# Performance work log

Measured on AMD Instinct MI355X. Metric: run time of the kernel, lower is better.

## Reference

```python
import jax, jax.numpy as jnp
import numpy as np

H, K, D = 4096, 16, 256  # hidden_dim, num_slots, slot_dim
BOT = 512                # decoder bottleneck
N_ITER = 3
EPS = 1e-5


def _ln(x, g, b):
    mu = jnp.mean(x, axis=-1, keepdims=True)
    var = jnp.var(x, axis=-1, keepdims=True)
    return (x - mu) * jax.lax.rsqrt(var + EPS) * g + b


def setup_inputs() -> dict:
    key = jax.random.key(0)
    ks = jax.random.split(key, 24)
    r = lambda i, shape, s=0.02: jax.random.normal(ks[i], shape, jnp.float32) * s
    inp = {
        "hidden_states": jax.random.normal(ks[0], (8, 4096, H), jnp.float32),
        "old_slots": jax.random.normal(ks[1], (8, K, D), jnp.float32) * 0.02,
        # SlotAttention params
        "in_w": r(2, (H, D)), "in_b": jnp.zeros((D,), jnp.float32),
        "ln_in_g": jnp.ones((D,), jnp.float32), "ln_in_b": jnp.zeros((D,), jnp.float32),
        "ln_s_g": jnp.ones((D,), jnp.float32), "ln_s_b": jnp.zeros((D,), jnp.float32),
        "ln_m_g": jnp.ones((D,), jnp.float32), "ln_m_b": jnp.zeros((D,), jnp.float32),
        "q_w": r(3, (D, D)), "k_w": r(4, (D, D)), "v_w": r(5, (D, D)),
        "mlp_w1": r(6, (D, 2 * D)), "mlp_b1": jnp.zeros((2 * D,), jnp.float32),
        "mlp_w2": r(7, (2 * D, D)), "mlp_b2": jnp.zeros((D,), jnp.float32),
        # ReconstructionDecoder params
        "dec_w1": r(8, (D, BOT)), "dec_b1": jnp.zeros((BOT,), jnp.float32),
        "dec_w2": r(9, (BOT, BOT)), "dec_b2": jnp.zeros((BOT,), jnp.float32),
        "dec_w3": r(10, (BOT, H)), "dec_b3": jnp.zeros((H,), jnp.float32),
    }
    return inp


def _forward(hidden_states, old_slots, in_w, in_b, ln_in_g, ln_in_b, ln_s_g, ln_s_b,
             ln_m_g, ln_m_b, q_w, k_w, v_w, mlp_w1, mlp_b1, mlp_w2, mlp_b2,
             dec_w1, dec_b1, dec_w2, dec_b2, dec_w3, dec_b3):
    B, T, _ = hidden_states.shape
    # subsample: 256 linspace over front + last 256 tokens (T > 512 branch)
    idx_front = jnp.linspace(0.0, T - 256, 256).astype(jnp.int32)  # torch long cast truncates; values are exact floor here
    idx_back = jnp.arange(T - 256, T, dtype=jnp.int32)
    idx = jnp.concatenate([idx_front, idx_back])
    sampled = hidden_states[:, idx, :]                 # [B, 512, H]

    x = _ln(sampled @ in_w + in_b, ln_in_g, ln_in_b)   # [B, 512, D]
    k = x @ k_w                                        # [B, 512, D]
    v = x @ v_w
    scale = D ** (-0.5)

    slots = old_slots                                  # [B, K, D]
    for _ in range(N_ITER):
        s = _ln(slots, ln_s_g, ln_s_b)
        q = s @ q_w
        logits = jnp.einsum('bkd,bnd->bkn', q, k) * scale
        attn = jax.nn.softmax(logits, axis=1)          # softmax over SLOT axis
        upd = jnp.einsum('bkn,bnd->bkd', attn, v)
        h = _ln(upd, ln_m_g, ln_m_b)
        slots = s + jax.nn.gelu(h @ mlp_w1 + mlp_b1, approximate=False) @ mlp_w2 + mlp_b2

    # reconstruction loss
    target = jax.lax.stop_gradient(jnp.mean(hidden_states, axis=1))     # [B, H]
    r = jax.nn.gelu(slots @ dec_w1 + dec_b1, approximate=False)
    r = jax.nn.gelu(r @ dec_w2 + dec_b2, approximate=False)
    r = r @ dec_w3 + dec_b3                                             # [B, K, H]
    recon = jnp.mean(r, axis=1)                                         # [B, H]
    recon_loss = jnp.mean((recon - target) ** 2)
    return slots, recon_loss


def reference(hidden_states, old_slots, in_w, in_b, ln_in_g, ln_in_b, ln_s_g, ln_s_b,
              ln_m_g, ln_m_b, q_w, k_w, v_w, mlp_w1, mlp_b1, mlp_w2, mlp_b2,
              dec_w1, dec_b1, dec_w2, dec_b2, dec_w3, dec_b3):
    return _forward(hidden_states, old_slots, in_w, in_b, ln_in_g, ln_in_b, ln_s_g,
                    ln_s_b, ln_m_g, ln_m_b, q_w, k_w, v_w, mlp_w1, mlp_b1, mlp_w2,
                    mlp_b2, dec_w1, dec_b1, dec_w2, dec_b2, dec_w3, dec_b3)
```

## Files before the change

kernel.cpp:

```cpp
#include <hip/hip_runtime.h>

typedef unsigned short u16;
typedef float f32x4 __attribute__((ext_vector_type(4)));
typedef __bf16 bf16x8 __attribute__((ext_vector_type(8)));
typedef u16 u16x4 __attribute__((ext_vector_type(4)));

__device__ __forceinline__ u16 f2bf(float f){
  union { float f; unsigned u; } x; x.f = f;
  return (u16)((x.u + 0x7FFFu + ((x.u >> 16) & 1u)) >> 16);
}
__device__ __forceinline__ float bf2f(u16 s){
  union { unsigned u; float f; } x; x.u = ((unsigned)s) << 16;
  return x.f;
}
__device__ __forceinline__ f32x4 mfma16(bf16x8 a, bf16x8 b, f32x4 c){
  return __builtin_amdgcn_mfma_f32_16x16x32_bf16(a, b, c, 0, 0, 0);
}
__device__ __forceinline__ float wred_sum(float x){
  #pragma unroll
  for (int m = 1; m < 64; m <<= 1) x += __shfl_xor(x, m);
  return x;
}
__device__ __forceinline__ float gelu_f(float v){
  return 0.5f * v * (1.0f + erff(v * 0.70710678118654752440f));
}
__device__ __forceinline__ int sample_idx(int r){
  return (r < 256) ? (3840 * r) / 255 : (3584 + r);
}

__global__ __launch_bounds__(256) void k_prep(
    const float* __restrict__ in_w, const float* __restrict__ q_w,
    const float* __restrict__ k_w, const float* __restrict__ v_w,
    const float* __restrict__ w1, const float* __restrict__ w2,
    u16* __restrict__ in_wT, u16* __restrict__ q_wT, u16* __restrict__ k_wT,
    u16* __restrict__ v_wT, u16* __restrict__ w1T, u16* __restrict__ w2T,
    float* __restrict__ loss_slot)
{
  __shared__ float tile[64][65];
  int id = blockIdx.x;
  const float* src; u16* dst; int R, C, t;
  if (id < 256)      { src=in_w; dst=in_wT; R=4096; C=256; t=id; }
  else if (id < 272) { src=q_w;  dst=q_wT;  R=256;  C=256; t=id-256; }
  else if (id < 288) { src=k_w;  dst=k_wT;  R=256;  C=256; t=id-272; }
  else if (id < 304) { src=v_w;  dst=v_wT;  R=256;  C=256; t=id-288; }
  else if (id < 336) { src=w1;   dst=w1T;   R=256;  C=512; t=id-304; }
  else               { src=w2;   dst=w2T;   R=512;  C=256; t=id-336; }
  int tC = C >> 6;
  int r0 = (t / tC) * 64, c0 = (t % tC) * 64;
  int tr = threadIdx.x >> 6, tc = threadIdx.x & 63;
  #pragma unroll
  for (int rr = tr; rr < 64; rr += 4)
    tile[rr][tc] = src[(size_t)(r0+rr)*C + c0 + tc];
  __syncthreads();
  #pragma unroll
  for (int cc = tr; cc < 64; cc += 4)
    dst[(size_t)(c0+cc)*R + r0 + tc] = f2bf(tile[tc][cc]);
  if (id == 0 && threadIdx.x == 0) *loss_slot = 0.f;
}

__global__ __launch_bounds__(256) void k_colsum(const float* __restrict__ hs,
                                                float* __restrict__ parts)
{
  int tc = blockIdx.x;
  int hb = blockIdx.y;
  int b  = blockIdx.z;
  int h0 = hb*1024 + threadIdx.x*4;
  const float* p = hs + ((size_t)b*4096 + (size_t)tc*64)*4096 + h0;
  f32x4 s = {0.f,0.f,0.f,0.f};
  for (int t = 0; t < 64; ++t)
    s += *reinterpret_cast<const f32x4*>(p + (size_t)t*4096);
  *reinterpret_cast<f32x4*>(parts + ((size_t)(b*64+tc) << 12) + h0) = s;
}

__global__ __launch_bounds__(256) void k_colsum2(const float* __restrict__ parts,
                                                 float* __restrict__ tgt)
{
  int i = blockIdx.x*256 + threadIdx.x;
  int b = i >> 12, h = i & 4095;
  float s = 0.f;
  for (int c = 0; c < 64; ++c) s += parts[((size_t)(b*64+c) << 12) + h];
  tgt[i] = s * (1.0f/4096.0f);
}

__global__ __launch_bounds__(256) void k_in_gemm_ln(
    const float* __restrict__ hs, const u16* __restrict__ in_wT,
    const float* __restrict__ in_b,
    const float* __restrict__ ln_g, const float* __restrict__ ln_b,
    u16* __restrict__ x_b)
{
  __shared__ float xt[16][260];
  const int lane = threadIdx.x & 63;
  const int w = threadIdx.x >> 6;
  const int c16 = lane & 15, g4 = lane >> 4;
  const int m0 = blockIdx.x * 16;
  const int row = m0 + c16;
  const int b = row >> 9;
  const int tok = row & 511;
  const int src = sample_idx(tok);
  const float* arow = hs + ((size_t)b*4096 + src)*4096 + g4*8;

  f32x4 acc[4];
  #pragma unroll
  for (int ct=0; ct<4; ++ct) acc[ct] = (f32x4){0.f,0.f,0.f,0.f};

  for (int k0 = 0; k0 < 4096; k0 += 32) {
    f32x4 a0 = *reinterpret_cast<const f32x4*>(arow + k0);
    f32x4 a1 = *reinterpret_cast<const f32x4*>(arow + k0 + 4);
    union { u16 u[8]; bf16x8 v; } af;
    #pragma unroll
    for (int i=0;i<4;++i){ af.u[i] = f2bf(a0[i]); af.u[4+i] = f2bf(a1[i]); }
    #pragma unroll
    for (int ct=0; ct<4; ++ct){
      int col = w*64 + ct*16 + c16;
      bf16x8 bf = *reinterpret_cast<const bf16x8*>(in_wT + (size_t)col*4096 + k0 + g4*8);
      acc[ct] = mfma16(af.v, bf, acc[ct]);
    }
  }
  #pragma unroll
  for (int ct=0; ct<4; ++ct){
    int col = w*64 + ct*16 + c16;
    float bias = in_b[col];
    #pragma unroll
    for (int i=0;i<4;++i) xt[g4*4+i][col] = acc[ct][i] + bias;
  }
  __syncthreads();
  #pragma unroll
  for (int rr=0; rr<4; ++rr){
    int r = 4*w + rr;
    f32x4 v = *reinterpret_cast<const f32x4*>(&xt[r][4*lane]);
    float s = v[0]+v[1]+v[2]+v[3];
    float q = v[0]*v[0]+v[1]*v[1]+v[2]*v[2]+v[3]*v[3];
    s = wred_sum(s); q = wred_sum(q);
    float mu = s*(1.0f/256.0f);
    float var = q*(1.0f/256.0f) - mu*mu;
    float rs = rsqrtf(var + 1e-5f);
    u16x4 pk;
    #pragma unroll
    for (int i=0;i<4;++i) pk[i] = f2bf((v[i]-mu)*rs*ln_g[4*lane+i] + ln_b[4*lane+i]);
    *reinterpret_cast<u16x4*>(x_b + (size_t)(m0 + r)*256 + 4*lane) = pk;
  }
}

__global__ __launch_bounds__(256) void k_kv(
    const u16* __restrict__ x_b, const u16* __restrict__ k_wT, const u16* __restrict__ v_wT,
    u16* __restrict__ k_out, u16* __restrict__ vT_out)
{
  const int lane = threadIdx.x & 63;
  const int w = threadIdx.x >> 6;
  const int c16 = lane & 15, g4 = lane >> 4;
  const int m0 = blockIdx.x * 16;
  const u16* aptr = x_b + (size_t)(m0 + c16)*256 + g4*8;
  f32x4 ak[4], av[4];
  #pragma unroll
  for (int ct=0; ct<4; ++ct){ ak[ct]=(f32x4){0.f,0.f,0.f,0.f}; av[ct]=(f32x4){0.f,0.f,0.f,0.f}; }
  #pragma unroll
  for (int kk=0; kk<8; ++kk){
    bf16x8 af = *reinterpret_cast<const bf16x8*>(aptr + kk*32);
    #pragma unroll
    for (int ct=0; ct<4; ++ct){
      int col = w*64 + ct*16 + c16;
      bf16x8 bk = *reinterpret_cast<const bf16x8*>(k_wT + (size_t)col*256 + kk*32 + g4*8);
      bf16x8 bv = *reinterpret_cast<const bf16x8*>(v_wT + (size_t)col*256 + kk*32 + g4*8);
      ak[ct] = mfma16(af, bk, ak[ct]);
      av[ct] = mfma16(af, bv, av[ct]);
    }
  }
  const int b = m0 >> 9;
  const int tok0 = (m0 & 511) + g4*4;
  #pragma unroll
  for (int ct=0; ct<4; ++ct){
    int col = w*64 + ct*16 + c16;
    #pragma unroll
    for (int i=0;i<4;++i)
      k_out[(size_t)(m0 + g4*4 + i)*256 + col] = f2bf(ak[ct][i]);
    u16x4 pk;
    #pragma unroll
    for (int i=0;i<4;++i) pk[i] = f2bf(av[ct][i]);
    *reinterpret_cast<u16x4*>(vT_out + ((size_t)(b*256 + col))*512 + tok0) = pk;
  }
}

__global__ __launch_bounds__(1024) void k_slots(
    const float* __restrict__ old_slots,
    const u16* __restrict__ k_b, const u16* __restrict__ vT_b,
    const u16* __restrict__ q_wT, const u16* __restrict__ w1T, const u16* __restrict__ w2T,
    const float* __restrict__ ln_s_g, const float* __restrict__ ln_s_b,
    const float* __restrict__ ln_m_g, const float* __restrict__ ln_m_b,
    const float* __restrict__ mlp_b1, const float* __restrict__ mlp_b2,
    float* __restrict__ out_slots)
{
  __shared__ u16 bufA[16*264];
  __shared__ u16 qS[16*264];
  __shared__ u16 wideS[16*520];
  __shared__ u16 updS[16*264];

  const int lane = threadIdx.x & 63;
  const int w    = threadIdx.x >> 6;
  const int c16  = lane & 15;
  const int g4   = lane >> 4;
  const int b    = blockIdx.x;

  const u16* kb = k_b  + (size_t)b * 512 * 256;
  const u16* vb = vT_b + (size_t)b * 256 * 512;

  float sl[4];
  {
    const float* p = old_slots + ((size_t)b*16 + w)*256 + 4*lane;
    #pragma unroll
    for (int i=0;i<4;++i) sl[i] = p[i];
  }
  float lsg[4], lsbv[4], lmg[4], lmb[4];
  #pragma unroll
  for (int i=0;i<4;++i){
    lsg[i]  = ln_s_g[4*lane+i];
    lsbv[i] = ln_s_b[4*lane+i];
    lmg[i]  = ln_m_g[4*lane+i];
    lmb[i]  = ln_m_b[4*lane+i];
  }
  const float b1a = mlp_b1[32*w + c16];
  const float b1b = mlp_b1[32*w + 16 + c16];
  const float b2c = mlp_b2[16*w + c16];
  float sv[4];

  for (int it = 0; it < 3; ++it) {
    {
      float s = sl[0]+sl[1]+sl[2]+sl[3];
      float q = sl[0]*sl[0]+sl[1]*sl[1]+sl[2]*sl[2]+sl[3]*sl[3];
      s = wred_sum(s); q = wred_sum(q);
      float mu = s * (1.0f/256.0f);
      float var = q * (1.0f/256.0f) - mu*mu;
      float rs = rsqrtf(var + 1e-5f);
      u16x4 pk;
      #pragma unroll
      for (int i=0;i<4;++i){ sv[i] = (sl[i]-mu)*rs*lsg[i] + lsbv[i]; pk[i] = f2bf(sv[i]); }
      *reinterpret_cast<u16x4*>(bufA + w*264 + 4*lane) = pk;
    }
    __syncthreads();

    {
      f32x4 acc = {0.f,0.f,0.f,0.f};
      #pragma unroll
      for (int kk = 0; kk < 8; ++kk) {
        bf16x8 af = *reinterpret_cast<const bf16x8*>(bufA + c16*264 + kk*32 + g4*8);
        bf16x8 bf = *reinterpret_cast<const bf16x8*>(q_wT + (size_t)(16*w + c16)*256 + kk*32 + g4*8);
        acc = mfma16(af, bf, acc);
      }
      #pragma unroll
      for (int i=0;i<4;++i) qS[(g4*4+i)*264 + 16*w + c16] = f2bf(acc[i]);
    }
    __syncthreads();

    {
      bf16x8 qf[8];
      #pragma unroll
      for (int kk=0;kk<8;++kk)
        qf[kk] = *reinterpret_cast<const bf16x8*>(qS + c16*264 + kk*32 + g4*8);
      #pragma unroll
      for (int ct=0; ct<2; ++ct) {
        int n0 = 32*w + 16*ct;
        f32x4 acc = {0.f,0.f,0.f,0.f};
        #pragma unroll
        for (int kk=0;kk<8;++kk){
          bf16x8 bf = *reinterpret_cast<const bf16x8*>(kb + (size_t)(n0 + c16)*256 + kk*32 + g4*8);
          acc = mfma16(qf[kk], bf, acc);
        }
        float t0 = acc[0]*0.0625f, t1 = acc[1]*0.0625f, t2 = acc[2]*0.0625f, t3 = acc[3]*0.0625f;
        float mx = fmaxf(fmaxf(t0,t1), fmaxf(t2,t3));
        mx = fmaxf(mx, __shfl_xor(mx,16));
        mx = fmaxf(mx, __shfl_xor(mx,32));
        float e0 = expf(t0-mx), e1 = expf(t1-mx), e2 = expf(t2-mx), e3 = expf(t3-mx);
        float ss = e0+e1+e2+e3;
        ss += __shfl_xor(ss,16);
        ss += __shfl_xor(ss,32);
        float inv = 1.0f/ss;
        wideS[(g4*4+0)*520 + n0 + c16] = f2bf(e0*inv);
        wideS[(g4*4+1)*520 + n0 + c16] = f2bf(e1*inv);
        wideS[(g4*4+2)*520 + n0 + c16] = f2bf(e2*inv);
        wideS[(g4*4+3)*520 + n0 + c16] = f2bf(e3*inv);
      }
    }
    __syncthreads();

    {
      f32x4 acc = {0.f,0.f,0.f,0.f};
      #pragma unroll
      for (int kk=0; kk<16; ++kk){
        bf16x8 af = *reinterpret_cast<const bf16x8*>(wideS + c16*520 + kk*32 + g4*8);
        bf16x8 bf = *reinterpret_cast<const bf16x8*>(vb + (size_t)(16*w + c16)*512 + kk*32 + g4*8);
        acc = mfma16(af, bf, acc);
      }
      #pragma unroll
      for (int i=0;i<4;++i) updS[(g4*4+i)*264 + 16*w + c16] = f2bf(acc[i]);
    }
    __syncthreads();

    {
      u16x4 up = *reinterpret_cast<const u16x4*>(updS + w*264 + 4*lane);
      float uv[4];
      #pragma unroll
      for (int i=0;i<4;++i) uv[i] = bf2f(up[i]);
      float s = uv[0]+uv[1]+uv[2]+uv[3];
      float q = uv[0]*uv[0]+uv[1]*uv[1]+uv[2]*uv[2]+uv[3]*uv[3];
      s = wred_sum(s); q = wred_sum(q);
      float mu = s*(1.0f/256.0f);
      float var = q*(1.0f/256.0f) - mu*mu;
      float rs = rsqrtf(var + 1e-5f);
      u16x4 pk;
      #pragma unroll
      for (int i=0;i<4;++i) pk[i] = f2bf((uv[i]-mu)*rs*lmg[i] + lmb[i]);
      *reinterpret_cast<u16x4*>(bufA + w*264 + 4*lane) = pk;
    }
    __syncthreads();

    {
      bf16x8 hf[8];
      #pragma unroll
      for (int kk=0;kk<8;++kk)
        hf[kk] = *reinterpret_cast<const bf16x8*>(bufA + c16*264 + kk*32 + g4*8);
      #pragma unroll
      for (int ct=0; ct<2; ++ct){
        int n0 = 32*w + 16*ct;
        float bb = ct ? b1b : b1a;
        f32x4 acc = {0.f,0.f,0.f,0.f};
        #pragma unroll
        for (int kk=0;kk<8;++kk){
          bf16x8 bf = *reinterpret_cast<const bf16x8*>(w1T + (size_t)(n0 + c16)*256 + kk*32 + g4*8);
          acc = mfma16(hf[kk], bf, acc);
        }
        #pragma unroll
        for (int i=0;i<4;++i)
          wideS[(g4*4+i)*520 + n0 + c16] = f2bf(gelu_f(acc[i] + bb));
      }
    }
    __syncthreads();

    {
      f32x4 acc = {0.f,0.f,0.f,0.f};
      #pragma unroll
      for (int kk=0; kk<16; ++kk){
        bf16x8 af = *reinterpret_cast<const bf16x8*>(wideS + c16*520 + kk*32 + g4*8);
        bf16x8 bf = *reinterpret_cast<const bf16x8*>(w2T + (size_t)(16*w + c16)*512 + kk*32 + g4*8);
        acc = mfma16(af, bf, acc);
      }
      #pragma unroll
      for (int i=0;i<4;++i) bufA[(g4*4+i)*264 + 16*w + c16] = f2bf(acc[i] + b2c);
    }
    __syncthreads();
    {
      u16x4 ns = *reinterpret_cast<const u16x4*>(bufA + w*264 + 4*lane);
      #pragma unroll
      for (int i=0;i<4;++i) sl[i] = sv[i] + bf2f(ns[i]);
    }
    __syncthreads();
  }

  {
    float* p = out_slots + ((size_t)b*16 + w)*256 + 4*lane;
    #pragma unroll
    for (int i=0;i<4;++i) p[i] = sl[i];
  }
}

__global__ __launch_bounds__(256) void k_dec(
    const float* __restrict__ slots, const float* __restrict__ w1, const float* __restrict__ b1,
    const float* __restrict__ w2, const float* __restrict__ b2, float* __restrict__ r2g)
{
  __shared__ float sr[256];
  __shared__ float r1[512];
  const int row = blockIdx.x;
  const int t = threadIdx.x;
  sr[t] = slots[(size_t)row*256 + t];
  __syncthreads();
  float a0 = b1[t], a1 = b1[t+256];
  for (int i=0;i<256;++i){
    float s = sr[i];
    a0 = fmaf(s, w1[(size_t)i*512 + t], a0);
    a1 = fmaf(s, w1[(size_t)i*512 + t + 256], a1);
  }
  r1[t] = gelu_f(a0); r1[t+256] = gelu_f(a1);
  __syncthreads();
  float c0 = b2[t], c1 = b2[t+256];
  for (int i=0;i<512;++i){
    float s = r1[i];
    c0 = fmaf(s, w2[(size_t)i*512 + t], c0);
    c1 = fmaf(s, w2[(size_t)i*512 + t + 256], c1);
  }
  r2g[(size_t)row*512 + t]       = gelu_f(c0);
  r2g[(size_t)row*512 + t + 256] = gelu_f(c1);
}

__global__ __launch_bounds__(256) void k_loss(
    const float* __restrict__ r2g, const float* __restrict__ w3, const float* __restrict__ b3,
    const float* __restrict__ tgt, float* __restrict__ loss)
{
  __shared__ float rb[512];
  __shared__ float red[4];
  const int hb = blockIdx.x;
  const int b  = blockIdx.y;
  const int t  = threadIdx.x;
  for (int j = t; j < 512; j += 256){
    float s = 0.f;
    #pragma unroll
    for (int k2=0;k2<16;++k2) s += r2g[(size_t)(b*16 + k2)*512 + j];
    rb[j] = s * (1.0f/16.0f);
  }
  __syncthreads();
  const int h = hb*1024 + t*4;
  f32x4 acc = *reinterpret_cast<const f32x4*>(b3 + h);
  for (int j=0;j<512;++j){
    f32x4 wv = *reinterpret_cast<const f32x4*>(w3 + (size_t)j*4096 + h);
    float rj = rb[j];
    acc[0] = fmaf(rj, wv[0], acc[0]);
    acc[1] = fmaf(rj, wv[1], acc[1]);
    acc[2] = fmaf(rj, wv[2], acc[2]);
    acc[3] = fmaf(rj, wv[3], acc[3]);
  }
  f32x4 tg = *reinterpret_cast<const f32x4*>(tgt + (size_t)b*4096 + h);
  float d0 = acc[0]-tg[0], d1 = acc[1]-tg[1], d2 = acc[2]-tg[2], d3 = acc[3]-tg[3];
  float loc = d0*d0 + d1*d1 + d2*d2 + d3*d3;
  loc = wred_sum(loc);
  const int lane = t & 63, wv_ = t >> 6;
  if (lane == 0) red[wv_] = loc;
  __syncthreads();
  if (t == 0){
    float s = (red[0]+red[1]+red[2]+red[3]) * (1.0f/32768.0f);
    atomicAdd(loss, s);
  }
}

extern "C" void kernel_launch(void* const* d_in, const int* in_sizes, int n_in,
                              void* d_out, int out_size, void* d_ws, size_t ws_size,
                              hipStream_t stream)
{
  const float* hs      = (const float*)d_in[0];
  const float* oslots  = (const float*)d_in[1];
  const float* in_w    = (const float*)d_in[2];
  const float* in_b    = (const float*)d_in[3];
  const float* ln_in_g = (const float*)d_in[4];
  const float* ln_in_b = (const float*)d_in[5];
  const float* ln_s_g  = (const float*)d_in[6];
  const float* ln_s_b  = (const float*)d_in[7];
  const float* ln_m_g  = (const float*)d_in[8];
  const float* ln_m_b  = (const float*)d_in[9];
  const float* q_w     = (const float*)d_in[10];
  const float* k_w     = (const float*)d_in[11];
  const float* v_w     = (const float*)d_in[12];
  const float* mlp_w1  = (const float*)d_in[13];
  const float* mlp_b1  = (const float*)d_in[14];
  const float* mlp_w2  = (const float*)d_in[15];
  const float* mlp_b2  = (const float*)d_in[16];
  const float* dec_w1  = (const float*)d_in[17];
  const float* dec_b1  = (const float*)d_in[18];
  const float* dec_w2  = (const float*)d_in[19];
  const float* dec_b2  = (const float*)d_in[20];
  const float* dec_w3  = (const float*)d_in[21];
  const float* dec_b3  = (const float*)d_in[22];

  char* ws = (char*)d_ws;
  size_t off = 0;
  auto alloc = [&](size_t bytes)->char*{
    char* p = ws + off; off = (off + bytes + 255) & ~(size_t)255; return p;
  };
  float* tgt   = (float*)alloc((size_t)32768*4);
  float* parts = (float*)alloc((size_t)8*64*4096*4);
  u16* in_wT = (u16*)alloc((size_t)256*4096*2);
  u16* q_wT  = (u16*)alloc((size_t)65536*2);
  u16* k_wT  = (u16*)alloc((size_t)65536*2);
  u16* v_wT  = (u16*)alloc((size_t)65536*2);
  u16* w1T   = (u16*)alloc((size_t)131072*2);
  u16* w2T   = (u16*)alloc((size_t)131072*2);
  u16* x_b   = (u16*)alloc((size_t)4096*256*2);
  u16* kk_b  = (u16*)alloc((size_t)4096*256*2);
  u16* vT_b  = (u16*)alloc((size_t)8*256*512*2);
  float* r2g = (float*)alloc((size_t)128*512*4);

  float* out_slots = (float*)d_out;
  float* out_loss  = out_slots + 32768;

  hipLaunchKernelGGL(k_prep, dim3(368), dim3(256), 0, stream,
      in_w, q_w, k_w, v_w, mlp_w1, mlp_w2, in_wT, q_wT, k_wT, v_wT, w1T, w2T, out_loss);
  hipLaunchKernelGGL(k_colsum, dim3(64,4,8), dim3(256), 0, stream, hs, parts);
  hipLaunchKernelGGL(k_colsum2, dim3(128), dim3(256), 0, stream, parts, tgt);
  hipLaunchKernelGGL(k_in_gemm_ln, dim3(256), dim3(256), 0, stream,
      hs, in_wT, in_b, ln_in_g, ln_in_b, x_b);
  hipLaunchKernelGGL(k_kv, dim3(256), dim3(256), 0, stream, x_b, k_wT, v_wT, kk_b, vT_b);
  hipLaunchKernelGGL(k_slots, dim3(8), dim3(1024), 0, stream,
      oslots, kk_b, vT_b, q_wT, w1T, w2T,
      ln_s_g, ln_s_b, ln_m_g, ln_m_b, mlp_b1, mlp_b2, out_slots);
  hipLaunchKernelGGL(k_dec, dim3(128), dim3(256), 0, stream,
      out_slots, dec_w1, dec_b1, dec_w2, dec_b2, r2g);
  hipLaunchKernelGGL(k_loss, dim3(4,8), dim3(256), 0, stream,
      r2g, dec_w3, dec_b3, tgt, out_loss);
}
```

Measured before the change: 1.079 ms.

## Widen input GEMM blocks, split loss GEMV over j, use native bf16 convert

The input projection kernel now runs 8 waves per block, each owning 32 output columns instead of 64, so more waves share the same A-row loads and latency is better hidden. The decoder-loss GEMV is split along the bottleneck dimension into 4 partial kernels (128 blocks instead of 32), followed by a separate reduction kernel that adds the partials and computes the squared error. f2bf now uses the compiler's native bf16 conversion instead of manual rounding. The cost is an extra launch and a partial buffer, and the rounding behaviour for NaN may differ slightly.

```diff
diff --git a/kernel.cpp b/kernel.cpp
--- a/kernel.cpp
+++ b/kernel.cpp
@@ -6,8 +6,9 @@
 typedef u16 u16x4 __attribute__((ext_vector_type(4)));
 
 __device__ __forceinline__ u16 f2bf(float f){
-  union { float f; unsigned u; } x; x.f = f;
-  return (u16)((x.u + 0x7FFFu + ((x.u >> 16) & 1u)) >> 16);
+  __bf16 h = (__bf16)f;
+  union { __bf16 h; u16 u; } x; x.h = h;
+  return x.u;
 }
 __device__ __forceinline__ float bf2f(u16 s){
   union { unsigned u; float f; } x; x.u = ((unsigned)s) << 16;
@@ -82,7 +83,7 @@
   tgt[i] = s * (1.0f/4096.0f);
 }
 
-__global__ __launch_bounds__(256) void k_in_gemm_ln(
+__global__ __launch_bounds__(512) void k_in_gemm_ln(
     const float* __restrict__ hs, const u16* __restrict__ in_wT,
     const float* __restrict__ in_b,
     const float* __restrict__ ln_g, const float* __restrict__ ln_b,
@@ -99,9 +100,9 @@
   const int src = sample_idx(tok);
   const float* arow = hs + ((size_t)b*4096 + src)*4096 + g4*8;
 
-  f32x4 acc[4];
-  #pragma unroll
-  for (int ct=0; ct<4; ++ct) acc[ct] = (f32x4){0.f,0.f,0.f,0.f};
+  f32x4 acc[2];
+  acc[0] = (f32x4){0.f,0.f,0.f,0.f};
+  acc[1] = (f32x4){0.f,0.f,0.f,0.f};
 
   for (int k0 = 0; k0 < 4096; k0 += 32) {
     f32x4 a0 = *reinterpret_cast<const f32x4*>(arow + k0);
@@ -110,23 +111,23 @@
     #pragma unroll
     for (int i=0;i<4;++i){ af.u[i] = f2bf(a0[i]); af.u[4+i] = f2bf(a1[i]); }
     #pragma unroll
-    for (int ct=0; ct<4; ++ct){
-      int col = w*64 + ct*16 + c16;
+    for (int ct=0; ct<2; ++ct){
+      int col = w*32 + ct*16 + c16;
       bf16x8 bf = *reinterpret_cast<const bf16x8*>(in_wT + (size_t)col*4096 + k0 + g4*8);
       acc[ct] = mfma16(af.v, bf, acc[ct]);
     }
   }
   #pragma unroll
-  for (int ct=0; ct<4; ++ct){
-    int col = w*64 + ct*16 + c16;
+  for (int ct=0; ct<2; ++ct){
+    int col = w*32 + ct*16 + c16;
     float bias = in_b[col];
     #pragma unroll
     for (int i=0;i<4;++i) xt[g4*4+i][col] = acc[ct][i] + bias;
   }
   __syncthreads();
   #pragma unroll
-  for (int rr=0; rr<4; ++rr){
-    int r = 4*w + rr;
+  for (int rr=0; rr<2; ++rr){
+    int r = 2*w + rr;
     f32x4 v = *reinterpret_cast<const f32x4*>(&xt[r][4*lane]);
     float s = v[0]+v[1]+v[2]+v[3];
     float q = v[0]*v[0]+v[1]*v[1]+v[2]*v[2]+v[3]*v[3];
@@ -389,40 +390,54 @@
   r2g[(size_t)row*512 + t + 256] = gelu_f(c1);
 }
 
-__global__ __launch_bounds__(256) void k_loss(
+__global__ __launch_bounds__(256) void k_loss_part(
     const float* __restrict__ r2g, const float* __restrict__ w3, const float* __restrict__ b3,
-    const float* __restrict__ tgt, float* __restrict__ loss)
-{
-  __shared__ float rb[512];
-  __shared__ float red[4];
+    float* __restrict__ rpart)
+{
+  __shared__ float rb[128];
   const int hb = blockIdx.x;
   const int b  = blockIdx.y;
+  const int jc = blockIdx.z;
   const int t  = threadIdx.x;
-  for (int j = t; j < 512; j += 256){
+  const int j0 = jc*128;
+  if (t < 128){
     float s = 0.f;
     #pragma unroll
-    for (int k2=0;k2<16;++k2) s += r2g[(size_t)(b*16 + k2)*512 + j];
-    rb[j] = s * (1.0f/16.0f);
+    for (int k2=0;k2<16;++k2) s += r2g[(size_t)(b*16 + k2)*512 + j0 + t];
+    rb[t] = s * (1.0f/16.0f);
   }
   __syncthreads();
   const int h = hb*1024 + t*4;
-  f32x4 acc = *reinterpret_cast<const f32x4*>(b3 + h);
-  for (int j=0;j<512;++j){
-    f32x4 wv = *reinterpret_cast<const f32x4*>(w3 + (size_t)j*4096 + h);
+  f32x4 acc;
+  if (jc == 0) acc = *reinterpret_cast<const f32x4*>(b3 + h);
+  else         acc = (f32x4){0.f,0.f,0.f,0.f};
+  for (int j=0;j<128;++j){
+    f32x4 wv = *reinterpret_cast<const f32x4*>(w3 + (size_t)(j0+j)*4096 + h);
     float rj = rb[j];
     acc[0] = fmaf(rj, wv[0], acc[0]);
     acc[1] = fmaf(rj, wv[1], acc[1]);
     acc[2] = fmaf(rj, wv[2], acc[2]);
     acc[3] = fmaf(rj, wv[3], acc[3]);
   }
-  f32x4 tg = *reinterpret_cast<const f32x4*>(tgt + (size_t)b*4096 + h);
-  float d0 = acc[0]-tg[0], d1 = acc[1]-tg[1], d2 = acc[2]-tg[2], d3 = acc[3]-tg[3];
-  float loc = d0*d0 + d1*d1 + d2*d2 + d3*d3;
-  loc = wred_sum(loc);
-  const int lane = t & 63, wv_ = t >> 6;
+  *reinterpret_cast<f32x4*>(rpart + (((size_t)jc*8 + b) << 12) + h) = acc;
+}
+
+__global__ __launch_bounds__(256) void k_loss_final(
+    const float* __restrict__ rpart, const float* __restrict__ tgt,
+    float* __restrict__ loss)
+{
+  __shared__ float red[4];
+  int i = blockIdx.x*256 + threadIdx.x;
+  int b = i >> 12, h = i & 4095;
+  float r = 0.f;
+  #pragma unroll
+  for (int jc=0; jc<4; ++jc) r += rpart[(((size_t)jc*8 + b) << 12) + h];
+  float d = r - tgt[i];
+  float loc = wred_sum(d*d);
+  const int lane = threadIdx.x & 63, wv_ = threadIdx.x >> 6;
   if (lane == 0) red[wv_] = loc;
   __syncthreads();
-  if (t == 0){
+  if (threadIdx.x == 0){
     float s = (red[0]+red[1]+red[2]+red[3]) * (1.0f/32768.0f);
     atomicAdd(loss, s);
   }
@@ -473,6 +488,7 @@
   u16* kk_b  = (u16*)alloc((size_t)4096*256*2);
   u16* vT_b  = (u16*)alloc((size_t)8*256*512*2);
   float* r2g = (float*)alloc((size_t)128*512*4);
+  float* rpart = (float*)alloc((size_t)4*8*4096*4);
 
   float* out_slots = (float*)d_out;
   float* out_loss  = out_slots + 32768;
@@ -481,7 +497,7 @@
       in_w, q_w, k_w, v_w, mlp_w1, mlp_w2, in_wT, q_wT, k_wT, v_wT, w1T, w2T, out_loss);
   hipLaunchKernelGGL(k_colsum, dim3(64,4,8), dim3(256), 0, stream, hs, parts);
   hipLaunchKernelGGL(k_colsum2, dim3(128), dim3(256), 0, stream, parts, tgt);
-  hipLaunchKernelGGL(k_in_gemm_ln, dim3(256), dim3(256), 0, stream,
+  hipLaunchKernelGGL(k_in_gemm_ln, dim3(256), dim3(512), 0, stream,
       hs, in_wT, in_b, ln_in_g, ln_in_b, x_b);
   hipLaunchKernelGGL(k_kv, dim3(256), dim3(256), 0, stream, x_b, k_wT, v_wT, kk_b, vT_b);
   hipLaunchKernelGGL(k_slots, dim3(8), dim3(1024), 0, stream,
@@ -489,6 +505,8 @@
       ln_s_g, ln_s_b, ln_m_g, ln_m_b, mlp_b1, mlp_b2, out_slots);
   hipLaunchKernelGGL(k_dec, dim3(128), dim3(256), 0, stream,
       out_slots, dec_w1, dec_b1, dec_w2, dec_b2, r2g);
-  hipLaunchKernelGGL(k_loss, dim3(4,8), dim3(256), 0, stream,
-      r2g, dec_w3, dec_b3, tgt, out_loss);
-}
+  hipLaunchKernelGGL(k_loss_part, dim3(4,8,4), dim3(256), 0, stream,
+      r2g, dec_w3, dec_b3, rpart);
+  hipLaunchKernelGGL(k_loss_final, dim3(128), dim3(256), 0, stream,
+      rpart, tgt, out_loss);
+}
```

New measurement: 1.086 ms. Within noise of the previous version (+0.7%).
